# Performance work log

Hardware: AMD Instinct MI355X
Metric: run time of the kernel (lower is better)

## Reference

```python
import jax, jax.numpy as jnp
import numpy as np

EMBED_DIM = 512
N_HEADS = 8
HEAD_DIM = EMBED_DIM // N_HEADS
MAX_GENES = 5000
SPARSITY_RATIO = 0.1
WINDOW = 20  # SparseAttention local window


def make_sparse_mask(key):
    # local band |i-j| <= window//2, plus random connections, plus diagonal
    idx = jnp.arange(MAX_GENES)
    mask = jnp.abs(idx[:, None] - idx[None, :]) <= (WINDOW // 2)
    n_random = int(SPARSITY_RATIO * MAX_GENES * MAX_GENES)
    k1, k2 = jax.random.split(key)
    ri = jax.random.randint(k1, (n_random,), 0, MAX_GENES)
    rj = jax.random.randint(k2, (n_random,), 0, MAX_GENES)
    mask = mask.at[ri, rj].set(True)
    mask = mask.at[idx, idx].set(True)
    return mask  # bool [MAX_GENES, MAX_GENES]


def setup_inputs() -> dict:
    key = jax.random.key(0)
    ks = jax.random.split(key, 10)
    B, S, E = 1, 4096, EMBED_DIM
    x = jax.random.normal(ks[0], (B, S, E), dtype=jnp.float32)
    init = lambda k: jax.random.normal(k, (E, E), dtype=jnp.float32) * 0.02
    return {
        "x": x,
        "Wq": init(ks[1]), "bq": jnp.zeros((E,), jnp.float32),
        "Wk": init(ks[2]), "bk": jnp.zeros((E,), jnp.float32),
        "Wv": init(ks[3]), "bv": jnp.zeros((E,), jnp.float32),
        "Wo": init(ks[4]), "bo": jnp.zeros((E,), jnp.float32),
        "mask": make_sparse_mask(ks[5]),
    }


def reference(x, Wq, bq, Wk, bk, Wv, bv, Wo, bo, mask):
    B, S, E = x.shape
    H, D = N_HEADS, HEAD_DIM
    # QKV projections (torch Linear: x @ W.T + b), split heads -> [B,H,S,D]
    Q = (x @ Wq.T + bq).reshape(B, S, H, D).transpose(0, 2, 1, 3)
    K = (x @ Wk.T + bk).reshape(B, S, H, D).transpose(0, 2, 1, 3)
    V = (x @ Wv.T + bv).reshape(B, S, H, D).transpose(0, 2, 1, 3)
    scale = 1.0 / jnp.sqrt(jnp.asarray(D, dtype=jnp.float32))
    scores = jnp.einsum('bhsd,bhtd->bhst', Q, K) * scale
    m = mask[:S, :S]  # static sparse pattern
    # original: scores*mask then masked_fill(mask==0, -inf) -> equivalent where
    scores = jnp.where(m[None, None], scores, -jnp.inf)
    w = jax.nn.softmax(scores, axis=-1)
    w = jnp.nan_to_num(w, nan=0.0)  # diag is always unmasked, but keep faithful
    out = jnp.einsum('bhst,bhtd->bhsd', w, V)
    out = out.transpose(0, 2, 1, 3).reshape(B, S, E)
    return out @ Wo.T + bo
```

## Files before the change

kernel.cpp:

```cpp
#include <hip/hip_runtime.h>
#include <hip/hip_bf16.h>
#include <stdint.h>

#define S 4096
#define E 512
#define H 8
#define D 64
#define MROW 5000
#define NSPLIT 2
#define KT_PER (S / 64 / NSPLIT)

typedef __hip_bfloat16 bf16;
typedef __attribute__((ext_vector_type(8))) short bf16x8;
typedef __attribute__((ext_vector_type(4))) float f32x4;

#define CMUL (0.125f * 1.4426950408889634f)

__global__ void sniff(const unsigned int* __restrict__ mask,
                      int* __restrict__ flag)
{
    int lane = threadIdx.x & 63;
    int hit = 0;
    for (int i = lane; i < 2048; i += 64) {
        unsigned int w = mask[i];
        if (w > 1u && (w & 0xFEFEFEFEu) == 0u) hit = 1;
    }
    unsigned long long b = __ballot(hit);
    if (lane == 0) { flag[1] = (b != 0ull) ? 1 : 0; flag[0] = 1; }
}

__global__ __launch_bounds__(256) void convert_all(
    const float* __restrict__ x,  const float* __restrict__ wq,
    const float* __restrict__ wk, const float* __restrict__ wv,
    const float* __restrict__ wo, const float* __restrict__ bq,
    const float* __restrict__ bk, const float* __restrict__ bv,
    const float* __restrict__ bo,
    bf16* __restrict__ xb, bf16* __restrict__ wcat, bf16* __restrict__ wob,
    bf16* __restrict__ bcat, bf16* __restrict__ bob)
{
    const float* srcs[9] = {x, wq, wk, wv, wo, bq, bk, bv, bo};
    bf16* dsts[9] = {xb, wcat, wcat + 262144, wcat + 524288, wob,
                     bcat, bcat + 512, bcat + 1024, bob};
    const int cnts[9] = {2097152, 262144, 262144, 262144, 262144,
                         512, 512, 512, 512};
    const int ngroups = (2097152 + 4 * 262144 + 4 * 512) / 4;
    for (int g = blockIdx.x * blockDim.x + threadIdx.x; g < ngroups;
         g += gridDim.x * blockDim.x) {
        int e = g * 4;
        int seg = 0;
        while (e >= cnts[seg]) { e -= cnts[seg]; ++seg; }
        float4 v = *(const float4*)(srcs[seg] + e);
        union { bf16 h[4]; uint2 u; } cv;
        cv.h[0] = (bf16)v.x; cv.h[1] = (bf16)v.y;
        cv.h[2] = (bf16)v.z; cv.h[3] = (bf16)v.w;
        *(uint2*)(dsts[seg] + e) = cv.u;
    }
}

__global__ __launch_bounds__(256) void pack_mask(const void* __restrict__ mask,
                                                 unsigned long long* __restrict__ bits,
                                                 const int* __restrict__ flag)
{
    const bool isbyte = flag[1] != 0;
    int wid   = (blockIdx.x * blockDim.x + threadIdx.x) >> 6;
    int lane  = threadIdx.x & 63;
    int nwav  = (gridDim.x * blockDim.x) >> 6;
    int total = S * (S / 64);
    for (int w = wid; w < total; w += nwav) {
        int row  = w >> 6;
        int word = w & 63;
        int col  = word * 64 + lane;
        unsigned int v;
        if (isbyte) v = ((const unsigned char*)mask)[(size_t)row * MROW + col];
        else        v = ((const unsigned int*)mask)[(size_t)row * MROW + col];
        unsigned long long b = __ballot(v != 0u);
        if (lane == 0) bits[(size_t)row * 64 + word] = b;
    }
}

__global__ __launch_bounds__(256) void gemm64(const bf16* __restrict__ A,
                                              const bf16* __restrict__ W,
                                              const bf16* __restrict__ bias,
                                              void* __restrict__ outv, int mode)
{
    __shared__ bf16 As[64][72];
    __shared__ bf16 Bs[64][72];
    const int tid  = threadIdx.x;
    const int wid  = tid >> 6, lane = tid & 63;
    const int quad = lane >> 4, l15 = lane & 15;
    const int nbase = blockIdx.x * 64;
    const int mbase = blockIdx.y * 64;
    const int m0 = wid * 16;

    f32x4 acc[4];
#pragma unroll
    for (int i = 0; i < 4; ++i) acc[i] = (f32x4){0.f, 0.f, 0.f, 0.f};

    for (int kt = 0; kt < E / 64; ++kt) {
        const int kb = kt * 64;
        __syncthreads();
#pragma unroll
        for (int i = 0; i < 2; ++i) {
            int slot = tid + i * 256;
            int row = slot >> 3, kg = slot & 7;
            *(uint4*)&As[row][kg * 8] = *(const uint4*)&A[(size_t)(mbase + row) * E + kb + kg * 8];
            *(uint4*)&Bs[row][kg * 8] = *(const uint4*)&W[(size_t)(nbase + row) * E + kb + kg * 8];
        }
        __syncthreads();
        bf16x8 a0 = *(bf16x8*)&As[m0 + l15][quad * 8];
        bf16x8 a1 = *(bf16x8*)&As[m0 + l15][32 + quad * 8];
#pragma unroll
        for (int nt = 0; nt < 4; ++nt) {
            bf16x8 b0 = *(bf16x8*)&Bs[nt * 16 + l15][quad * 8];
            bf16x8 b1 = *(bf16x8*)&Bs[nt * 16 + l15][32 + quad * 8];
            acc[nt] = __builtin_amdgcn_mfma_f32_16x16x32_bf16(a0, b0, acc[nt], 0, 0, 0);
            acc[nt] = __builtin_amdgcn_mfma_f32_16x16x32_bf16(a1, b1, acc[nt], 0, 0, 0);
        }
    }
#pragma unroll
    for (int nt = 0; nt < 4; ++nt) {
        int col = nbase + nt * 16 + l15;
        float bv = (float)bias[col];
#pragma unroll
        for (int r = 0; r < 4; ++r) {
            int row = mbase + m0 + quad * 4 + r;
            float v = acc[nt][r] + bv;
            if (mode == 0) {
                int t = col >> 9, hh = (col >> 6) & 7, d = col & 63;
                if (t == 0) v *= CMUL;
                ((bf16*)outv)[((size_t)t * H + hh) * S * D + (size_t)row * D + d] = (bf16)v;
            } else {
                ((float*)outv)[(size_t)row * E + col] = v;
            }
        }
    }
}

__global__ __launch_bounds__(256) void attn(const bf16* __restrict__ Qp,
                                            const bf16* __restrict__ Kp,
                                            const bf16* __restrict__ Vp,
                                            const unsigned long long* __restrict__ bits,
                                            float* __restrict__ Opart,
                                            float* __restrict__ Lpart)
{
    __shared__ bf16 Qs[64][72];
    __shared__ bf16 Ks[64][72];
    __shared__ bf16 Vts[64][72];
    __shared__ bf16 Ps[4][16][64];

    const int tid  = threadIdx.x;
    const int wid  = tid >> 6, lane = tid & 63;
    const int quad = lane >> 4, l15 = lane & 15;
    const int qt = blockIdx.x, h = blockIdx.y, split = blockIdx.z;
    const int qbase = qt * 64;
    const int m0 = wid * 16;
    const bf16* Qh = Qp + (size_t)h * S * D;
    const bf16* Kh = Kp + (size_t)h * S * D;
    const bf16* Vh = Vp + (size_t)h * S * D;

    const int krow0 = tid >> 3,        kkg = tid & 7;
    const int krow1 = (tid + 256) >> 3;
    const int vt0 = (tid & 31) * 2,    vd0 = (tid >> 5) * 8;

#pragma unroll
    for (int i = 0; i < 2; ++i) {
        int slot = tid + i * 256;
        int row = slot >> 3, kg = slot & 7;
        *(uint4*)&Qs[row][kg * 8] = *(const uint4*)&Qh[(size_t)(qbase + row) * D + kg * 8];
    }
    __syncthreads();
    bf16x8 aq0 = *(bf16x8*)&Qs[m0 + l15][quad * 8];
    bf16x8 aq1 = *(bf16x8*)&Qs[m0 + l15][32 + quad * 8];

    bf16x8 bl;
    {
        union { short s; bf16 b; } one; one.b = (bf16)1.0f;
        short v = (l15 == 0) ? one.s : (short)0;
#pragma unroll
        for (int j = 0; j < 8; ++j) bl[j] = v;
    }

    f32x4 o[4];
#pragma unroll
    for (int dt = 0; dt < 4; ++dt) o[dt] = (f32x4){0.f, 0.f, 0.f, 0.f};
    f32x4 accl = (f32x4){0.f, 0.f, 0.f, 0.f};

    const int kt0 = split * KT_PER, kt1 = kt0 + KT_PER;

    uint4 kq0, kq1, vq0, vq1;
    {
        const int kbase = kt0 * 64;
        kq0 = *(const uint4*)&Kh[(size_t)(kbase + krow0) * D + kkg * 8];
        kq1 = *(const uint4*)&Kh[(size_t)(kbase + krow1) * D + kkg * 8];
        vq0 = *(const uint4*)&Vh[(size_t)(kbase + vt0) * D + vd0];
        vq1 = *(const uint4*)&Vh[(size_t)(kbase + vt0 + 1) * D + vd0];
    }

    const int pkey = ((l15 >> 1) & 7);
    for (int kt = kt0; kt < kt1; ++kt) {
        __syncthreads();
        *(uint4*)&Ks[krow0][kkg * 8] = kq0;
        *(uint4*)&Ks[krow1][kkg * 8] = kq1;
        {
            const unsigned short* p0 = (const unsigned short*)&vq0;
            const unsigned short* p1 = (const unsigned short*)&vq1;
#pragma unroll
            for (int j = 0; j < 8; ++j) {
                unsigned int pk = (unsigned int)p0[j] | ((unsigned int)p1[j] << 16);
                *(unsigned int*)&Vts[vd0 + j][vt0] = pk;
            }
        }
        if (kt + 1 < kt1) {
            const int kb2 = (kt + 1) * 64;
            kq0 = *(const uint4*)&Kh[(size_t)(kb2 + krow0) * D + kkg * 8];
            kq1 = *(const uint4*)&Kh[(size_t)(kb2 + krow1) * D + kkg * 8];
            vq0 = *(const uint4*)&Vh[(size_t)(kb2 + vt0) * D + vd0];
            vq1 = *(const uint4*)&Vh[(size_t)(kb2 + vt0 + 1) * D + vd0];
        }
        unsigned long long mw[4];
#pragma unroll
        for (int r = 0; r < 4; ++r) {
            int row = qbase + m0 + quad * 4 + r;
            mw[r] = bits[(size_t)row * 64 + kt];
        }
        __syncthreads();

        f32x4 sc[4];
        {
            f32x4 z = (f32x4){0.f, 0.f, 0.f, 0.f};
#pragma unroll
            for (int nt = 0; nt < 4; ++nt) {
                bf16x8 b0 = *(bf16x8*)&Ks[nt * 16 + l15][quad * 8];
                bf16x8 b1 = *(bf16x8*)&Ks[nt * 16 + l15][32 + quad * 8];
                sc[nt] = __builtin_amdgcn_mfma_f32_16x16x32_bf16(aq0, b0, z, 0, 0, 0);
                sc[nt] = __builtin_amdgcn_mfma_f32_16x16x32_bf16(aq1, b1, sc[nt], 0, 0, 0);
            }
        }
#pragma unroll
        for (int r = 0; r < 4; ++r) {
            unsigned long long sh = mw[r] >> l15;
            int row = quad * 4 + r;
            int key = ((row >> 1) & 7) << 3;
#pragma unroll
            for (int nt = 0; nt < 4; ++nt) {
                float p = __builtin_amdgcn_exp2f(sc[nt][r]);
                bool ok = (sh >> (nt * 16)) & 1ull;
                p = ok ? p : 0.f;
                Ps[wid][row][(nt * 16 + l15) ^ key] = (bf16)p;
            }
        }
        bf16x8 ap0 = *(bf16x8*)&Ps[wid][l15][(quad ^ pkey) * 8];
        bf16x8 ap1 = *(bf16x8*)&Ps[wid][l15][((quad + 4) ^ pkey) * 8];
        accl = __builtin_amdgcn_mfma_f32_16x16x32_bf16(ap0, bl, accl, 0, 0, 0);
        accl = __builtin_amdgcn_mfma_f32_16x16x32_bf16(ap1, bl, accl, 0, 0, 0);
#pragma unroll
        for (int dt = 0; dt < 4; ++dt) {
            bf16x8 bv0 = *(bf16x8*)&Vts[dt * 16 + l15][quad * 8];
            bf16x8 bv1 = *(bf16x8*)&Vts[dt * 16 + l15][32 + quad * 8];
            o[dt] = __builtin_amdgcn_mfma_f32_16x16x32_bf16(ap0, bv0, o[dt], 0, 0, 0);
            o[dt] = __builtin_amdgcn_mfma_f32_16x16x32_bf16(ap1, bv1, o[dt], 0, 0, 0);
        }
    }
    float* Op = Opart + (size_t)(split * H + h) * S * D;
    float* Lp = Lpart + (size_t)(split * H + h) * S;
#pragma unroll
    for (int r = 0; r < 4; ++r) {
        int row = qbase + m0 + quad * 4 + r;
        if (l15 == 0) Lp[row] = accl[r];
#pragma unroll
        for (int dt = 0; dt < 4; ++dt)
            Op[(size_t)row * D + dt * 16 + l15] = o[dt][r];
    }
}

__global__ __launch_bounds__(256) void combine(const float* __restrict__ Opart,
                                               const float* __restrict__ Lpart,
                                               bf16* __restrict__ Ow)
{
    int g = blockIdx.x * 256 + threadIdx.x;
    int e = g * 4;
    int row = e >> 9;
    int c = e & 511;
    int h = c >> 6, d = c & 63;
    size_t base = ((size_t)h * S + row) * D + d;
    const size_t oh = (size_t)H * S * D;
    float4 a = *(const float4*)(Opart + base);
    float4 b = *(const float4*)(Opart + oh + base);
    float l = Lpart[(size_t)h * S + row] + Lpart[(size_t)H * S + (size_t)h * S + row];
    float inv = (l > 0.f) ? 1.f / l : 0.f;
    union { bf16 x[4]; uint2 u; } ov;
    ov.x[0] = (bf16)((a.x + b.x) * inv);
    ov.x[1] = (bf16)((a.y + b.y) * inv);
    ov.x[2] = (bf16)((a.z + b.z) * inv);
    ov.x[3] = (bf16)((a.w + b.w) * inv);
    *(uint2*)(Ow + (size_t)row * E + c) = ov.u;
}

extern "C" void kernel_launch(void* const* d_in, const int* in_sizes, int n_in,
                              void* d_out, int out_size, void* d_ws, size_t ws_size,
                              hipStream_t stream)
{
    char* ws = (char*)d_ws;
    const size_t MB = (size_t)1 << 20;
    bf16* Qw   = (bf16*)(ws + 0 * MB);
    bf16* Kw   = (bf16*)(ws + 4 * MB);
    bf16* Vw   = (bf16*)(ws + 8 * MB);
    bf16* Ow   = (bf16*)(ws + 12 * MB);
    unsigned long long* bits = (unsigned long long*)(ws + 16 * MB);
    bf16* xb   = (bf16*)(ws + 18 * MB);
    bf16* Wcat = (bf16*)(ws + 22 * MB);
    bf16* Wob  = (bf16*)(ws + 24 * MB);
    bf16* bcat = (bf16*)(ws + 25 * MB);
    bf16* bob  = (bf16*)(ws + 25 * MB + 8192);
    int*  flag = (int*)(ws + 25 * MB + 16384);
    float* Opart = (float*)(ws + 26 * MB);
    float* Lpart = (float*)(ws + 42 * MB);

    hipLaunchKernelGGL(sniff, dim3(1), dim3(64), 0, stream,
                       (const unsigned int*)d_in[9], flag);
    hipLaunchKernelGGL(convert_all, dim3(1024), dim3(256), 0, stream,
                       (const float*)d_in[0], (const float*)d_in[1],
                       (const float*)d_in[3], (const float*)d_in[5],
                       (const float*)d_in[7], (const float*)d_in[2],
                       (const float*)d_in[4], (const float*)d_in[6],
                       (const float*)d_in[8],
                       xb, Wcat, Wob, bcat, bob);
    hipLaunchKernelGGL(pack_mask, dim3(1024), dim3(256), 0, stream, d_in[9], bits, flag);
    hipLaunchKernelGGL(gemm64, dim3(24, 64), dim3(256), 0, stream, xb, Wcat, bcat, (void*)Qw, 0);
    hipLaunchKernelGGL(attn, dim3(64, 8, NSPLIT), dim3(256), 0, stream,
                       Qw, Kw, Vw, bits, Opart, Lpart);
    hipLaunchKernelGGL(combine, dim3(2048), dim3(256), 0, stream, Opart, Lpart, Ow);
    hipLaunchKernelGGL(gemm64, dim3(8, 64), dim3(256), 0, stream, Ow, Wob, bob, d_out, 1);
}
```

Measured before the change: 315.2 us.

## Use 128-row query tiles with 512 threads and a variable key split count

The attention kernel now handles 128 query rows per block with 8 waves sharing each K/V tile, which halves K/V global loads per query. Shared memory is packed into one buffer, with Ps aliased onto Qs. The key-split count becomes a runtime value: 4 when the workspace is large enough, otherwise 2, and the combine kernel loops over the splits. The aim is to raise K/V reuse while keeping enough blocks in flight. In exchange, the per-element V transpose stores get narrower and combine reads more partial buffers.

```diff
diff --git a/kernel.cpp b/kernel.cpp
--- a/kernel.cpp
+++ b/kernel.cpp
@@ -7,8 +7,6 @@
 #define H 8
 #define D 64
 #define MROW 5000
-#define NSPLIT 2
-#define KT_PER (S / 64 / NSPLIT)
 
 typedef __hip_bfloat16 bf16;
 typedef __attribute__((ext_vector_type(8))) short bf16x8;
@@ -136,35 +134,36 @@
     }
 }
 
-__global__ __launch_bounds__(256) void attn(const bf16* __restrict__ Qp,
-                                            const bf16* __restrict__ Kp,
-                                            const bf16* __restrict__ Vp,
-                                            const unsigned long long* __restrict__ bits,
-                                            float* __restrict__ Opart,
-                                            float* __restrict__ Lpart)
-{
-    __shared__ bf16 Qs[64][72];
-    __shared__ bf16 Ks[64][72];
-    __shared__ bf16 Vts[64][72];
-    __shared__ bf16 Ps[4][16][64];
+__global__ __launch_bounds__(512, 8) void attn(const bf16* __restrict__ Qp,
+                                               const bf16* __restrict__ Kp,
+                                               const bf16* __restrict__ Vp,
+                                               const unsigned long long* __restrict__ bits,
+                                               float* __restrict__ Opart,
+                                               float* __restrict__ Lpart,
+                                               int ktper)
+{
+    __shared__ __align__(16) char smem[36864];
+    bf16 (*Ks)[72]  = (bf16(*)[72])smem;
+    bf16 (*Vts)[72] = (bf16(*)[72])(smem + 9216);
+    bf16 (*Qs)[72]  = (bf16(*)[72])(smem + 18432);
+    bf16 (*Ps)[16][64] = (bf16(*)[16][64])(smem + 18432);
 
     const int tid  = threadIdx.x;
     const int wid  = tid >> 6, lane = tid & 63;
     const int quad = lane >> 4, l15 = lane & 15;
     const int qt = blockIdx.x, h = blockIdx.y, split = blockIdx.z;
-    const int qbase = qt * 64;
+    const int qbase = qt * 128;
     const int m0 = wid * 16;
     const bf16* Qh = Qp + (size_t)h * S * D;
     const bf16* Kh = Kp + (size_t)h * S * D;
     const bf16* Vh = Vp + (size_t)h * S * D;
 
-    const int krow0 = tid >> 3,        kkg = tid & 7;
-    const int krow1 = (tid + 256) >> 3;
-    const int vt0 = (tid & 31) * 2,    vd0 = (tid >> 5) * 8;
+    const int krow = tid >> 3, kkg = tid & 7;
+    const int vt0 = tid & 63,  vd0 = (tid >> 6) * 8;
 
 #pragma unroll
     for (int i = 0; i < 2; ++i) {
-        int slot = tid + i * 256;
+        int slot = tid + i * 512;
         int row = slot >> 3, kg = slot & 7;
         *(uint4*)&Qs[row][kg * 8] = *(const uint4*)&Qh[(size_t)(qbase + row) * D + kg * 8];
     }
@@ -185,37 +184,28 @@
     for (int dt = 0; dt < 4; ++dt) o[dt] = (f32x4){0.f, 0.f, 0.f, 0.f};
     f32x4 accl = (f32x4){0.f, 0.f, 0.f, 0.f};
 
-    const int kt0 = split * KT_PER, kt1 = kt0 + KT_PER;
-
-    uint4 kq0, kq1, vq0, vq1;
+    const int kt0 = split * ktper, kt1 = kt0 + ktper;
+
+    uint4 kq, vq;
     {
         const int kbase = kt0 * 64;
-        kq0 = *(const uint4*)&Kh[(size_t)(kbase + krow0) * D + kkg * 8];
-        kq1 = *(const uint4*)&Kh[(size_t)(kbase + krow1) * D + kkg * 8];
-        vq0 = *(const uint4*)&Vh[(size_t)(kbase + vt0) * D + vd0];
-        vq1 = *(const uint4*)&Vh[(size_t)(kbase + vt0 + 1) * D + vd0];
+        kq = *(const uint4*)&Kh[(size_t)(kbase + krow) * D + kkg * 8];
+        vq = *(const uint4*)&Vh[(size_t)(kbase + vt0) * D + vd0];
     }
 
     const int pkey = ((l15 >> 1) & 7);
     for (int kt = kt0; kt < kt1; ++kt) {
         __syncthreads();
-        *(uint4*)&Ks[krow0][kkg * 8] = kq0;
-        *(uint4*)&Ks[krow1][kkg * 8] = kq1;
+        *(uint4*)&Ks[krow][kkg * 8] = kq;
         {
-            const unsigned short* p0 = (const unsigned short*)&vq0;
-            const unsigned short* p1 = (const unsigned short*)&vq1;
-#pragma unroll
-            for (int j = 0; j < 8; ++j) {
-                unsigned int pk = (unsigned int)p0[j] | ((unsigned int)p1[j] << 16);
-                *(unsigned int*)&Vts[vd0 + j][vt0] = pk;
-            }
+            const bf16* pv = (const bf16*)&vq;
+#pragma unroll
+            for (int j = 0; j < 8; ++j) Vts[vd0 + j][vt0] = pv[j];
         }
         if (kt + 1 < kt1) {
             const int kb2 = (kt + 1) * 64;
-            kq0 = *(const uint4*)&Kh[(size_t)(kb2 + krow0) * D + kkg * 8];
-            kq1 = *(const uint4*)&Kh[(size_t)(kb2 + krow1) * D + kkg * 8];
-            vq0 = *(const uint4*)&Vh[(size_t)(kb2 + vt0) * D + vd0];
-            vq1 = *(const uint4*)&Vh[(size_t)(kb2 + vt0 + 1) * D + vd0];
+            kq = *(const uint4*)&Kh[(size_t)(kb2 + krow) * D + kkg * 8];
+            vq = *(const uint4*)&Vh[(size_t)(kb2 + vt0) * D + vd0];
         }
         unsigned long long mw[4];
 #pragma unroll
@@ -275,7 +265,7 @@
 
 __global__ __launch_bounds__(256) void combine(const float* __restrict__ Opart,
                                                const float* __restrict__ Lpart,
-                                               bf16* __restrict__ Ow)
+                                               bf16* __restrict__ Ow, int nsplit)
 {
     int g = blockIdx.x * 256 + threadIdx.x;
     int e = g * 4;
@@ -284,15 +274,18 @@
     int h = c >> 6, d = c & 63;
     size_t base = ((size_t)h * S + row) * D + d;
     const size_t oh = (size_t)H * S * D;
-    float4 a = *(const float4*)(Opart + base);
-    float4 b = *(const float4*)(Opart + oh + base);
-    float l = Lpart[(size_t)h * S + row] + Lpart[(size_t)H * S + (size_t)h * S + row];
+    float ax = 0.f, ay = 0.f, az = 0.f, aw = 0.f, l = 0.f;
+    for (int s = 0; s < nsplit; ++s) {
+        float4 a = *(const float4*)(Opart + (size_t)s * oh + base);
+        ax += a.x; ay += a.y; az += a.z; aw += a.w;
+        l += Lpart[(size_t)s * H * S + (size_t)h * S + row];
+    }
     float inv = (l > 0.f) ? 1.f / l : 0.f;
     union { bf16 x[4]; uint2 u; } ov;
-    ov.x[0] = (bf16)((a.x + b.x) * inv);
-    ov.x[1] = (bf16)((a.y + b.y) * inv);
-    ov.x[2] = (bf16)((a.z + b.z) * inv);
-    ov.x[3] = (bf16)((a.w + b.w) * inv);
+    ov.x[0] = (bf16)(ax * inv);
+    ov.x[1] = (bf16)(ay * inv);
+    ov.x[2] = (bf16)(az * inv);
+    ov.x[3] = (bf16)(aw * inv);
     *(uint2*)(Ow + (size_t)row * E + c) = ov.u;
 }
 
@@ -314,7 +307,10 @@
     bf16* bob  = (bf16*)(ws + 25 * MB + 8192);
     int*  flag = (int*)(ws + 25 * MB + 16384);
     float* Opart = (float*)(ws + 26 * MB);
-    float* Lpart = (float*)(ws + 42 * MB);
+
+    int nsplit = (ws_size >= 60 * MB) ? 4 : 2;
+    int ktper  = (S / 64) / nsplit;
+    float* Lpart = (float*)(ws + 26 * MB + (size_t)nsplit * 8 * MB);
 
     hipLaunchKernelGGL(sniff, dim3(1), dim3(64), 0, stream,
                        (const unsigned int*)d_in[9], flag);
@@ -327,8 +323,8 @@
                        xb, Wcat, Wob, bcat, bob);
     hipLaunchKernelGGL(pack_mask, dim3(1024), dim3(256), 0, stream, d_in[9], bits, flag);
     hipLaunchKernelGGL(gemm64, dim3(24, 64), dim3(256), 0, stream, xb, Wcat, bcat, (void*)Qw, 0);
-    hipLaunchKernelGGL(attn, dim3(64, 8, NSPLIT), dim3(256), 0, stream,
-                       Qw, Kw, Vw, bits, Opart, Lpart);
-    hipLaunchKernelGGL(combine, dim3(2048), dim3(256), 0, stream, Opart, Lpart, Ow);
+    hipLaunchKernelGGL(attn, dim3(S / 128, H, nsplit), dim3(512), 0, stream,
+                       Qw, Kw, Vw, bits, Opart, Lpart, ktper);
+    hipLaunchKernelGGL(combine, dim3(2048), dim3(256), 0, stream, Opart, Lpart, Ow, nsplit);
     hipLaunchKernelGGL(gemm64, dim3(8, 64), dim3(256), 0, stream, Ow, Wob, bob, d_out, 1);
 }
```

Result: slower. 484.7 us (+53.8%).
